# Optimization experiments

Measured on AMD Instinct MI355X. Metric: run time of the kernel, lower is better.

The kernel has to match this reference:

```python
import jax, jax.numpy as jnp
import numpy as np

TOP_K = 2


def setup_inputs() -> dict:
    key = jax.random.key(0)
    k1, k2 = jax.random.split(key)
    hidden_states = jax.random.normal(k1, (4, 8192, 4096), dtype=jnp.float32)
    # xavier_uniform for Linear(4096 -> 64): bound = sqrt(6/(fan_in+fan_out))
    bound = float(np.sqrt(6.0 / (4096 + 64)))
    gate_w = jax.random.uniform(k2, (64, 4096), dtype=jnp.float32, minval=-bound, maxval=bound)
    return {"hidden_states": hidden_states, "gate_w": gate_w}


def reference(hidden_states, gate_w):
    # Flatten [B, S, H] -> [T, H]
    H = hidden_states.shape[-1]
    x = hidden_states.reshape(-1, H)
    # Gate projection: [T, H] @ [H, E] -> [T, E]
    router_logits = jnp.einsum('th,eh->te', x, gate_w)
    # Top-k expert selection (eval mode: no noise)
    top_k_logits, top_k_indices = jax.lax.top_k(router_logits, TOP_K)
    # Normalize selected weights with a softmax over the k logits
    top_k_weights = jax.nn.softmax(top_k_logits, axis=-1)
    return top_k_weights, top_k_indices, router_logits
```

## Files before the change

kernel.cpp:

```cpp
#include <hip/hip_runtime.h>


#define NT    512
#define TT    32768
#define HD    4096
#define NE    64
#define BKT   32
#define NKT   128
#define KCH   2
#define NCH   (NKT / KCH)
#define BROWS 128
#define LDSBUF_U4 1536

typedef __attribute__((ext_vector_type(8))) short bf16x8;
typedef __attribute__((ext_vector_type(4))) float f32x4;

#define MFMA __builtin_amdgcn_mfma_f32_16x16x32_bf16

__device__ __forceinline__ bf16x8 u2b(uint4 u) {
  return __builtin_bit_cast(bf16x8, u);
}

__device__ __forceinline__ void tsplit8(float4 a, float4 b,
                                        uint4& o0, uint4& o1, uint4& o2) {
  float f[8] = {a.x, a.y, a.z, a.w, b.x, b.y, b.z, b.w};
  unsigned p0[4], p1[4], p2[4];
#pragma unroll
  for (int j = 0; j < 4; ++j) {
    float x0 = f[2 * j], x1 = f[2 * j + 1];
    unsigned u0 = __float_as_uint(x0) & 0xffff0000u;
    unsigned u1 = __float_as_uint(x1) & 0xffff0000u;
    float r0 = x0 - __uint_as_float(u0);
    float r1 = x1 - __uint_as_float(u1);
    unsigned v0 = __float_as_uint(r0) & 0xffff0000u;
    unsigned v1 = __float_as_uint(r1) & 0xffff0000u;
    float s0 = r0 - __uint_as_float(v0);
    float s1 = r1 - __uint_as_float(v1);
    p0[j] = (u0 >> 16) | u1;
    p1[j] = (v0 >> 16) | v1;
    p2[j] = (__float_as_uint(s0) >> 16) | (__float_as_uint(s1) & 0xffff0000u);
  }
  o0 = make_uint4(p0[0], p0[1], p0[2], p0[3]);
  o1 = make_uint4(p1[0], p1[1], p1[2], p1[3]);
  o2 = make_uint4(p2[0], p2[1], p2[2], p2[3]);
}

__global__ __launch_bounds__(256)
void prepack_w_kernel(const float* __restrict__ W, uint4* __restrict__ Bp) {
  const int t  = blockIdx.x * 256 + threadIdx.x;
  const int e  = t >> 9;
  const int c8 = t & 511;
  const int k0 = c8 * 8;
  const float4* wp = (const float4*)(W + (size_t)e * HD + k0);
  uint4 o0, o1, o2;
  tsplit8(wp[0], wp[1], o0, o1, o2);
  const int ts = k0 >> 5;
  const int lg = (k0 >> 3) & 3;
  const int f  = e >> 4;
  const int ln = lg * 16 + (e & 15);
  Bp[(((ts * 3 + 0) * 4 + f) << 6) + ln] = o0;
  Bp[(((ts * 3 + 1) * 4 + f) << 6) + ln] = o1;
  Bp[(((ts * 3 + 2) * 4 + f) << 6) + ln] = o2;
}

__global__ __launch_bounds__(NT, 2)
void router_frag_kernel(const float* __restrict__ A, const uint4* __restrict__ Bp,
                        float* __restrict__ outw, float* __restrict__ outi,
                        float* __restrict__ outl) {
  __shared__ __align__(16) uint4 smem[2 * LDSBUF_U4];

  const int tid  = threadIdx.x;
  const int bm   = blockIdx.x;
  const int lane = tid & 63;
  const int w    = tid >> 6;
  const int l15  = lane & 15;
  const int lg   = lane >> 4;

  const int row = bm * BROWS + w * 16 + l15;
  const float* pa = A + (size_t)row * HD + lg * 8;

  const uint4* bsrc = Bp + w * 192 + lane;

  f32x4 acc0 = {0.f,0.f,0.f,0.f}, acc1 = {0.f,0.f,0.f,0.f};
  f32x4 acc2 = {0.f,0.f,0.f,0.f}, acc3 = {0.f,0.f,0.f,0.f};

  uint4 st0, st1, st2;

#define SLOAD(CH) { \
    const uint4* q_ = bsrc + (size_t)(CH) * LDSBUF_U4; \
    st0 = q_[0]; st1 = q_[64]; st2 = q_[128]; }

#define SWRITE(BUFI) { \
    uint4* d_ = smem + (BUFI) * LDSBUF_U4 + w * 192 + lane; \
    d_[0] = st0; d_[64] = st1; d_[128] = st2; }

#define FRAG(T4, F, ACC, A0_, A1_, A2_) { \
    const bf16x8 q0_ = bbx[(((T4) * 3 + 0) * 4 + (F)) * 64 + lane]; \
    const bf16x8 q1_ = bbx[(((T4) * 3 + 1) * 4 + (F)) * 64 + lane]; \
    const bf16x8 q2_ = bbx[(((T4) * 3 + 2) * 4 + (F)) * 64 + lane]; \
    ACC = MFMA(A0_, q2_, ACC, 0, 0, 0); \
    ACC = MFMA(A1_, q1_, ACC, 0, 0, 0); \
    ACC = MFMA(A2_, q0_, ACC, 0, 0, 0); \
    ACC = MFMA(A0_, q1_, ACC, 0, 0, 0); \
    ACC = MFMA(A1_, q0_, ACC, 0, 0, 0); \
    ACC = MFMA(A0_, q0_, ACC, 0, 0, 0); }

#define STEP(T4, AX0, AX1, AY0, AY1) { \
    int tn_ = t0s + (T4) + 1; if (tn_ >= NKT) tn_ = NKT - 1; \
    const float4* ap_ = (const float4*)(pa + (size_t)tn_ * BKT); \
    AY0 = ap_[0]; AY1 = ap_[1]; \
    uint4 x0_, x1_, x2_; \
    tsplit8(AX0, AX1, x0_, x1_, x2_); \
    const bf16x8 a0_ = u2b(x0_), a1_ = u2b(x1_), a2_ = u2b(x2_); \
    FRAG(T4, 0, acc0, a0_, a1_, a2_) \
    FRAG(T4, 1, acc1, a0_, a1_, a2_) \
    FRAG(T4, 2, acc2, a0_, a1_, a2_) \
    FRAG(T4, 3, acc3, a0_, a1_, a2_) }

  SLOAD(0)
  SWRITE(0)
  float4 aX0, aX1, aY0, aY1;
  { const float4* ap = (const float4*)pa; aX0 = ap[0]; aX1 = ap[1]; }
  __syncthreads();

#pragma unroll 1
  for (int c = 0; c < NCH; ++c) {
    const bf16x8* bbx = (const bf16x8*)(smem + (c & 1) * LDSBUF_U4);
    const int t0s = c * KCH;
    const bool more = (c + 1 < NCH);
    if (more) { SLOAD(c + 1) }
    __builtin_amdgcn_sched_barrier(0);
    STEP(0, aX0, aX1, aY0, aY1)
    STEP(1, aY0, aY1, aX0, aX1)
    if (more) { SWRITE((c + 1) & 1) }
    __syncthreads();
  }

  const int tb = bm * BROWS;
  float* lf = (float*)smem;
  const int rbase = w * 16 + lg * 4;

#define EPO(F, ACC) { \
    _Pragma("unroll") \
    for (int r = 0; r < 4; ++r) { \
      int tl = rbase + r; int e = (F) * 16 + l15; float v = ACC[r]; \
      outl[(size_t)(tb + tl) * NE + e] = v; \
      lf[tl * 65 + e] = v; \
    } }
  EPO(0, acc0) EPO(1, acc1) EPO(2, acc2) EPO(3, acc3)
#undef EPO

  __syncthreads();

  if (tid < BROWS) {
    const int t = tid;
    float m1 = -1e30f, m2 = -1e30f;
    int i1 = 0, i2 = 0;
#pragma unroll
    for (int e = 0; e < NE; ++e) {
      float v = lf[t * 65 + e];
      if (v > m1)      { m2 = m1; i2 = i1; m1 = v; i1 = e; }
      else if (v > m2) { m2 = v; i2 = e; }
    }
    float e2  = expf(m2 - m1);
    float inv = 1.0f / (1.0f + e2);
    outw[(size_t)(tb + t) * 2 + 0] = inv;
    outw[(size_t)(tb + t) * 2 + 1] = e2 * inv;
    outi[(size_t)(tb + t) * 2 + 0] = (float)i1;
    outi[(size_t)(tb + t) * 2 + 1] = (float)i2;
  }
}

#define PROD1(AM0, AM1, BS0, BS1) \
    acc00 = MFMA(AM0, BS0, acc00, 0, 0, 0); \
    acc01 = MFMA(AM0, BS1, acc01, 0, 0, 0); \
    acc10 = MFMA(AM1, BS0, acc10, 0, 0, 0); \
    acc11 = MFMA(AM1, BS1, acc11, 0, 0, 0);

__global__ __launch_bounds__(256, 2)
void topk_router_lds(const float* __restrict__ A, const float* __restrict__ W,
                     float* __restrict__ outw, float* __restrict__ outi,
                     float* __restrict__ outl) {
  __shared__ __align__(16) unsigned char smem[49152];
  const int tid  = threadIdx.x;
  const int bm   = blockIdx.x;
  const int lane = tid & 63;
  const int wid  = tid >> 6;
  const int wr   = wid >> 1;
  const int wc   = wid & 1;
  const int l15  = lane & 15;
  const int lg   = lane >> 4;
  const int s_r  = tid >> 2;
  const int s_cb = (tid & 3) << 3;
  const float* aball = A + (size_t)(bm * 64 + s_r) * HD + s_cb;
  const float* bball = W + (size_t)s_r * HD + s_cb;
  const unsigned wswz  = ((unsigned)((s_r >> 1) & 3)) << 4;
  const unsigned wbyte = (unsigned)(s_r * 64) + (((unsigned)(s_cb * 2)) ^ wswz);
  f32x4 acc00 = {0.f,0.f,0.f,0.f}, acc01 = {0.f,0.f,0.f,0.f};
  f32x4 acc10 = {0.f,0.f,0.f,0.f}, acc11 = {0.f,0.f,0.f,0.f};
  float4 aE0, aE1, bE0, bE1, aO0, aO1, bO0, bO1;
#define LOADS(T, A0, A1, B0, B1) { \
    const float4* ap = (const float4*)(aball + (size_t)(T) * BKT); \
    A0 = ap[0]; A1 = ap[1]; \
    const float4* bp = (const float4*)(bball + (size_t)(T) * BKT); \
    B0 = bp[0]; B1 = bp[1]; }
#define CONVW2(BB, A0, A1, B0, B1) { \
    uint4 o0, o1, o2; \
    tsplit8(A0, A1, o0, o1, o2); \
    *(uint4*)(smem + (BB) +     0 + wbyte) = o0; \
    *(uint4*)(smem + (BB) +  4096 + wbyte) = o1; \
    *(uint4*)(smem + (BB) +  8192 + wbyte) = o2; \
    tsplit8(B0, B1, o0, o1, o2); \
    *(uint4*)(smem + (BB) + 12288 + wbyte) = o0; \
    *(uint4*)(smem + (BB) + 16384 + wbyte) = o1; \
    *(uint4*)(smem + (BB) + 20480 + wbyte) = o2; }
  auto compute = [&](int bb) {
    bf16x8 a0m0, a0m1, a1m0, a1m1, a2m0, a2m1;
    bf16x8 b0n0, b0n1, b1n0, b1n1, b2n0, b2n1;
    const unsigned kb = (unsigned)(lg * 16);
#define LDA(SI, MI, DST) { \
    int row = wr * 32 + (MI) * 16 + l15; \
    DST = *(const bf16x8*)(smem + bb + (SI) * 4096 + row * 64 + \
          (kb ^ ((((unsigned)row >> 1) & 3) << 4))); }
#define LDB(SI, NI, DST) { \
    int row = wc * 32 + (NI) * 16 + l15; \
    DST = *(const bf16x8*)(smem + bb + 12288 + (SI) * 4096 + row * 64 + \
          (kb ^ ((((unsigned)row >> 1) & 3) << 4))); }
    LDA(0, 0, a0m0) LDA(0, 1, a0m1)
    LDA(1, 0, a1m0) LDA(1, 1, a1m1)
    LDA(2, 0, a2m0) LDA(2, 1, a2m1)
    LDB(0, 0, b0n0) LDB(0, 1, b0n1)
    LDB(1, 0, b1n0) LDB(1, 1, b1n1)
    LDB(2, 0, b2n0) LDB(2, 1, b2n1)
#undef LDA
#undef LDB
    PROD1(a0m0, a0m1, b2n0, b2n1)
    PROD1(a1m0, a1m1, b1n0, b1n1)
    PROD1(a2m0, a2m1, b0n0, b0n1)
    PROD1(a0m0, a0m1, b1n0, b1n1)
    PROD1(a1m0, a1m1, b0n0, b0n1)
    PROD1(a0m0, a0m1, b0n0, b0n1)
  };
  LOADS(0, aE0, aE1, bE0, bE1)
  LOADS(1, aO0, aO1, bO0, bO1)
  CONVW2(0, aE0, aE1, bE0, bE1)
  __syncthreads();
#pragma unroll 1
  for (int kk = 0; kk < NKT; kk += 2) {
    if (kk + 2 < NKT) { LOADS(kk + 2, aE0, aE1, bE0, bE1) }
    __builtin_amdgcn_sched_barrier(0);
    compute(0);
    CONVW2(24576, aO0, aO1, bO0, bO1)
    __syncthreads();
    if (kk + 3 < NKT) { LOADS(kk + 3, aO0, aO1, bO0, bO1) }
    __builtin_amdgcn_sched_barrier(0);
    compute(24576);
    if (kk + 2 < NKT) { CONVW2(0, aE0, aE1, bE0, bE1) }
    __syncthreads();
  }
  const int t0 = bm * 64;
  float* lf2 = (float*)smem;
#define EPI(MI, NI, ACC) \
  { _Pragma("unroll") \
    for (int r = 0; r < 4; ++r) { \
      int tl = wr * 32 + (MI) * 16 + lg * 4 + r; \
      int e  = wc * 32 + (NI) * 16 + l15; \
      float v = ACC[r]; \
      outl[(size_t)(t0 + tl) * NE + e] = v; \
      lf2[tl * 65 + e] = v; \
    } }
  EPI(0, 0, acc00) EPI(0, 1, acc01) EPI(1, 0, acc10) EPI(1, 1, acc11)
#undef EPI
  __syncthreads();
  if (tid < 64) {
    const int t = tid;
    float m1 = -1e30f, m2 = -1e30f;
    int i1 = 0, i2 = 0;
#pragma unroll
    for (int e = 0; e < NE; ++e) {
      float v = lf2[t * 65 + e];
      if (v > m1)      { m2 = m1; i2 = i1; m1 = v; i1 = e; }
      else if (v > m2) { m2 = v; i2 = e; }
    }
    float e2  = expf(m2 - m1);
    float inv = 1.0f / (1.0f + e2);
    outw[(size_t)(t0 + t) * 2 + 0] = inv;
    outw[(size_t)(t0 + t) * 2 + 1] = e2 * inv;
    outi[(size_t)(t0 + t) * 2 + 0] = (float)i1;
    outi[(size_t)(t0 + t) * 2 + 1] = (float)i2;
  }
}

extern "C" void kernel_launch(void* const* d_in, const int* in_sizes, int n_in,
                              void* d_out, int out_size, void* d_ws, size_t ws_size,
                              hipStream_t stream) {
  (void)in_sizes; (void)n_in; (void)out_size;
  const float* A = (const float*)d_in[0];
  const float* W = (const float*)d_in[1];
  float* outw = (float*)d_out;
  float* outi = (float*)d_out + 2 * TT;
  float* outl = (float*)d_out + 4 * TT;

  const size_t need = (size_t)NKT * 3 * 4 * 1024;
  if (ws_size >= need) {
    hipLaunchKernelGGL(prepack_w_kernel, dim3(128), dim3(256), 0, stream,
                       W, (uint4*)d_ws);
    hipLaunchKernelGGL(router_frag_kernel, dim3(TT / BROWS), dim3(NT), 0, stream,
                       A, (const uint4*)d_ws, outw, outi, outl);
  } else {
    hipLaunchKernelGGL(topk_router_lds, dim3(TT / 64), dim3(256), 0, stream,
                       A, W, outw, outi, outl);
  }
}
```

Baseline: 197.5 us.

## Stream activations into LDS via global_load_lds DMA with 2x2 warp tiling

Replaces the per-wave direct-register activation loads with asynchronous global-to-LDS DMA of 64-row activation tiles, double-buffered in LDS. The weight fragments now come straight from global memory into registers, and each wave computes a 32x32 output tile. The goal is to overlap the HBM streaming of activations with MFMA work and to cut the register-staging overhead. In exchange the block shrinks to 256 threads with 64 rows, padded LDS rows and more complex addressing, and the bf16x3 split moves to data read from LDS.

```diff
diff --git a/kernel.cpp b/kernel.cpp
--- a/kernel.cpp
+++ b/kernel.cpp
@@ -1,24 +1,27 @@
 #include <hip/hip_runtime.h>
 
 
-#define NT    512
+#define NT    256
 #define TT    32768
 #define HD    4096
 #define NE    64
 #define BKT   32
 #define NKT   128
-#define KCH   2
-#define NCH   (NKT / KCH)
-#define BROWS 128
-#define LDSBUF_U4 1536
+#define BUFB  25600
+#define ALIM  ((size_t)TT * HD * 4 - 16)
 
 typedef __attribute__((ext_vector_type(8))) short bf16x8;
 typedef __attribute__((ext_vector_type(4))) float f32x4;
 
 #define MFMA __builtin_amdgcn_mfma_f32_16x16x32_bf16
 
-__device__ __forceinline__ bf16x8 u2b(uint4 u) {
-  return __builtin_bit_cast(bf16x8, u);
+__device__ __forceinline__ bf16x8 u2b(uint4 u) { return __builtin_bit_cast(bf16x8, u); }
+__device__ __forceinline__ float4 b4f(uint4 u) { return __builtin_bit_cast(float4, u); }
+
+__device__ __forceinline__ void gload_lds16(const void* g, void* l) {
+  __builtin_amdgcn_global_load_lds(
+      (const __attribute__((address_space(1))) void*)g,
+      (__attribute__((address_space(3))) void*)l, 16, 0, 0);
 }
 
 __device__ __forceinline__ void tsplit8(float4 a, float4 b,
@@ -49,8 +52,7 @@
 void prepack_w_kernel(const float* __restrict__ W, uint4* __restrict__ Bp) {
   const int t  = blockIdx.x * 256 + threadIdx.x;
   const int e  = t >> 9;
-  const int c8 = t & 511;
-  const int k0 = c8 * 8;
+  const int k0 = (t & 511) * 8;
   const float4* wp = (const float4*)(W + (size_t)e * HD + k0);
   uint4 o0, o1, o2;
   tsplit8(wp[0], wp[1], o0, o1, o2);
@@ -63,96 +65,128 @@
   Bp[(((ts * 3 + 2) * 4 + f) << 6) + ln] = o2;
 }
 
+#define PROD1(AM0, AM1, BN0, BN1) \
+    acc00 = MFMA(AM0, BN0, acc00, 0, 0, 0); \
+    acc01 = MFMA(AM0, BN1, acc01, 0, 0, 0); \
+    acc10 = MFMA(AM1, BN0, acc10, 0, 0, 0); \
+    acc11 = MFMA(AM1, BN1, acc11, 0, 0, 0);
+
 __global__ __launch_bounds__(NT, 2)
-void router_frag_kernel(const float* __restrict__ A, const uint4* __restrict__ Bp,
-                        float* __restrict__ outw, float* __restrict__ outi,
-                        float* __restrict__ outl) {
-  __shared__ __align__(16) uint4 smem[2 * LDSBUF_U4];
+void router_dma_kernel(const float* __restrict__ A, const uint4* __restrict__ Bp,
+                       float* __restrict__ outw, float* __restrict__ outi,
+                       float* __restrict__ outl) {
+  __shared__ __align__(16) unsigned char smem[2 * BUFB];
 
   const int tid  = threadIdx.x;
   const int bm   = blockIdx.x;
   const int lane = tid & 63;
   const int w    = tid >> 6;
+  const int wr   = w >> 1;
+  const int wc   = w & 1;
   const int l15  = lane & 15;
   const int lg   = lane >> 4;
 
-  const int row = bm * BROWS + w * 16 + l15;
-  const float* pa = A + (size_t)row * HD + lg * 8;
-
-  const uint4* bsrc = Bp + w * 192 + lane;
-
-  f32x4 acc0 = {0.f,0.f,0.f,0.f}, acc1 = {0.f,0.f,0.f,0.f};
-  f32x4 acc2 = {0.f,0.f,0.f,0.f}, acc3 = {0.f,0.f,0.f,0.f};
-
-  uint4 st0, st1, st2;
-
-#define SLOAD(CH) { \
-    const uint4* q_ = bsrc + (size_t)(CH) * LDSBUF_U4; \
-    st0 = q_[0]; st1 = q_[64]; st2 = q_[128]; }
-
-#define SWRITE(BUFI) { \
-    uint4* d_ = smem + (BUFI) * LDSBUF_U4 + w * 192 + lane; \
-    d_[0] = st0; d_[64] = st1; d_[128] = st2; }
-
-#define FRAG(T4, F, ACC, A0_, A1_, A2_) { \
-    const bf16x8 q0_ = bbx[(((T4) * 3 + 0) * 4 + (F)) * 64 + lane]; \
-    const bf16x8 q1_ = bbx[(((T4) * 3 + 1) * 4 + (F)) * 64 + lane]; \
-    const bf16x8 q2_ = bbx[(((T4) * 3 + 2) * 4 + (F)) * 64 + lane]; \
-    ACC = MFMA(A0_, q2_, ACC, 0, 0, 0); \
-    ACC = MFMA(A1_, q1_, ACC, 0, 0, 0); \
-    ACC = MFMA(A2_, q0_, ACC, 0, 0, 0); \
-    ACC = MFMA(A0_, q1_, ACC, 0, 0, 0); \
-    ACC = MFMA(A1_, q0_, ACC, 0, 0, 0); \
-    ACC = MFMA(A0_, q0_, ACC, 0, 0, 0); }
-
-#define STEP(T4, AX0, AX1, AY0, AY1) { \
-    int tn_ = t0s + (T4) + 1; if (tn_ >= NKT) tn_ = NKT - 1; \
-    const float4* ap_ = (const float4*)(pa + (size_t)tn_ * BKT); \
-    AY0 = ap_[0]; AY1 = ap_[1]; \
-    uint4 x0_, x1_, x2_; \
-    tsplit8(AX0, AX1, x0_, x1_, x2_); \
-    const bf16x8 a0_ = u2b(x0_), a1_ = u2b(x1_), a2_ = u2b(x2_); \
-    FRAG(T4, 0, acc0, a0_, a1_, a2_) \
-    FRAG(T4, 1, acc1, a0_, a1_, a2_) \
-    FRAG(T4, 2, acc2, a0_, a1_, a2_) \
-    FRAG(T4, 3, acc3, a0_, a1_, a2_) }
-
-  SLOAD(0)
-  SWRITE(0)
-  float4 aX0, aX1, aY0, aY1;
-  { const float4* ap = (const float4*)pa; aX0 = ap[0]; aX1 = ap[1]; }
+  const char* Abytes = (const char*)A;
+
+  size_t srcoff[7];
+#pragma unroll
+  for (int j = 0; j < 7; ++j) {
+    int ii = j * 4 + w;
+    int f  = ii * 1024 + lane * 16;
+    int r  = f / 400, rb = f % 400;
+    srcoff[j] = (size_t)(bm * 64 + r) * (HD * 4) + (size_t)(rb < 384 ? rb : 0);
+  }
+
+#define DMA_ISSUE(CT, BOFF) { \
+    _Pragma("unroll") \
+    for (int j = 0; j < 7; ++j) { \
+      int ii = j * 4 + w; \
+      if (ii < 25) { \
+        size_t off = srcoff[j] + (size_t)(CT) * 384; \
+        if (off > ALIM) off -= (size_t)(HD * 4); \
+        gload_lds16(Abytes + off, smem + (BOFF) + ii * 1024); \
+      } \
+    } \
+    __builtin_amdgcn_sched_barrier(0); }
+
+  const int row0b = (wr * 32 + l15) * 400;
+  const int row1b = row0b + 16 * 400;
+  const int lgb   = lg * 32;
+
+  const uint4* pbB = Bp + wc * 128 + lane;
+
+  f32x4 acc00 = {0.f,0.f,0.f,0.f}, acc01 = {0.f,0.f,0.f,0.f};
+  f32x4 acc10 = {0.f,0.f,0.f,0.f}, acc11 = {0.f,0.f,0.f,0.f};
+
+  uint4 bA0f0, bA0f1, bA1f0, bA1f1, bA2f0, bA2f1;
+  uint4 bB0f0, bB0f1, bB1f0, bB1f1, bB2f0, bB2f1;
+
+#define LOADB(SET, G) { \
+    const uint4* q_ = pbB + (size_t)(G) * 768; \
+    SET##0f0 = q_[0];   SET##0f1 = q_[64]; \
+    SET##1f0 = q_[256]; SET##1f1 = q_[320]; \
+    SET##2f0 = q_[512]; SET##2f1 = q_[576]; }
+
+#define BSTEP(BOFF, S, BU, BL, GN, DOLOAD) { \
+    if (DOLOAD) { LOADB(BL, GN) } \
+    uint4 rA0lo = *(const uint4*)(smem + (BOFF) + row0b + (S) * 128 + lgb); \
+    uint4 rA0hi = *(const uint4*)(smem + (BOFF) + row0b + (S) * 128 + lgb + 16); \
+    uint4 rA1lo = *(const uint4*)(smem + (BOFF) + row1b + (S) * 128 + lgb); \
+    uint4 rA1hi = *(const uint4*)(smem + (BOFF) + row1b + (S) * 128 + lgb + 16); \
+    uint4 x0, x1, x2, y0, y1, y2; \
+    tsplit8(b4f(rA0lo), b4f(rA0hi), x0, x1, x2); \
+    tsplit8(b4f(rA1lo), b4f(rA1hi), y0, y1, y2); \
+    const bf16x8 a0m0 = u2b(x0), a1m0 = u2b(x1), a2m0 = u2b(x2); \
+    const bf16x8 a0m1 = u2b(y0), a1m1 = u2b(y1), a2m1 = u2b(y2); \
+    PROD1(a0m0, a0m1, u2b(BU##2f0), u2b(BU##2f1)) \
+    PROD1(a1m0, a1m1, u2b(BU##1f0), u2b(BU##1f1)) \
+    PROD1(a2m0, a2m1, u2b(BU##0f0), u2b(BU##0f1)) \
+    PROD1(a0m0, a0m1, u2b(BU##1f0), u2b(BU##1f1)) \
+    PROD1(a1m0, a1m1, u2b(BU##0f0), u2b(BU##0f1)) \
+    PROD1(a0m0, a0m1, u2b(BU##0f0), u2b(BU##0f1)) }
+
+  DMA_ISSUE(0, 0)
+  LOADB(bA, 0)
   __syncthreads();
 
 #pragma unroll 1
-  for (int c = 0; c < NCH; ++c) {
-    const bf16x8* bbx = (const bf16x8*)(smem + (c & 1) * LDSBUF_U4);
-    const int t0s = c * KCH;
-    const bool more = (c + 1 < NCH);
-    if (more) { SLOAD(c + 1) }
-    __builtin_amdgcn_sched_barrier(0);
-    STEP(0, aX0, aX1, aY0, aY1)
-    STEP(1, aY0, aY1, aX0, aX1)
-    if (more) { SWRITE((c + 1) & 1) }
+  for (int ot = 0; ot < 21; ++ot) {
+    const int g0 = ot * 6;
+    DMA_ISSUE(2 * ot + 1, BUFB)
+    BSTEP(0, 0, bA, bB, g0 + 1, true)
+    BSTEP(0, 1, bB, bA, g0 + 2, true)
+    BSTEP(0, 2, bA, bB, g0 + 3, true)
     __syncthreads();
-  }
-
-  const int tb = bm * BROWS;
+    DMA_ISSUE(2 * ot + 2, 0)
+    BSTEP(BUFB, 0, bB, bA, g0 + 4, true)
+    BSTEP(BUFB, 1, bA, bB, g0 + 5, true)
+    BSTEP(BUFB, 2, bB, bA, g0 + 6, true)
+    __syncthreads();
+  }
+
+  BSTEP(0, 0, bA, bB, 127, true)
+  BSTEP(0, 1, bB, bA, 0, false)
+
+  const int t0 = bm * 64;
   float* lf = (float*)smem;
-  const int rbase = w * 16 + lg * 4;
-
-#define EPO(F, ACC) { \
-    _Pragma("unroll") \
+
+  __syncthreads();
+
+#define EPO(MI, NI, ACC) \
+  { _Pragma("unroll") \
     for (int r = 0; r < 4; ++r) { \
-      int tl = rbase + r; int e = (F) * 16 + l15; float v = ACC[r]; \
-      outl[(size_t)(tb + tl) * NE + e] = v; \
+      int tl = wr * 32 + (MI) * 16 + lg * 4 + r; \
+      int e  = wc * 32 + (NI) * 16 + l15; \
+      float v = ACC[r]; \
+      outl[(size_t)(t0 + tl) * NE + e] = v; \
       lf[tl * 65 + e] = v; \
     } }
-  EPO(0, acc0) EPO(1, acc1) EPO(2, acc2) EPO(3, acc3)
+  EPO(0, 0, acc00) EPO(0, 1, acc01) EPO(1, 0, acc10) EPO(1, 1, acc11)
 #undef EPO
 
   __syncthreads();
 
-  if (tid < BROWS) {
+  if (tid < 64) {
     const int t = tid;
     float m1 = -1e30f, m2 = -1e30f;
     int i1 = 0, i2 = 0;
@@ -164,18 +198,12 @@
     }
     float e2  = expf(m2 - m1);
     float inv = 1.0f / (1.0f + e2);
-    outw[(size_t)(tb + t) * 2 + 0] = inv;
-    outw[(size_t)(tb + t) * 2 + 1] = e2 * inv;
-    outi[(size_t)(tb + t) * 2 + 0] = (float)i1;
-    outi[(size_t)(tb + t) * 2 + 1] = (float)i2;
-  }
-}
-
-#define PROD1(AM0, AM1, BS0, BS1) \
-    acc00 = MFMA(AM0, BS0, acc00, 0, 0, 0); \
-    acc01 = MFMA(AM0, BS1, acc01, 0, 0, 0); \
-    acc10 = MFMA(AM1, BS0, acc10, 0, 0, 0); \
-    acc11 = MFMA(AM1, BS1, acc11, 0, 0, 0);
+    outw[(size_t)(t0 + t) * 2 + 0] = inv;
+    outw[(size_t)(t0 + t) * 2 + 1] = e2 * inv;
+    outi[(size_t)(t0 + t) * 2 + 0] = (float)i1;
+    outi[(size_t)(t0 + t) * 2 + 1] = (float)i2;
+  }
+}
 
 __global__ __launch_bounds__(256, 2)
 void topk_router_lds(const float* __restrict__ A, const float* __restrict__ W,
@@ -305,7 +333,7 @@
   if (ws_size >= need) {
     hipLaunchKernelGGL(prepack_w_kernel, dim3(128), dim3(256), 0, stream,
                        W, (uint4*)d_ws);
-    hipLaunchKernelGGL(router_frag_kernel, dim3(TT / BROWS), dim3(NT), 0, stream,
+    hipLaunchKernelGGL(router_dma_kernel, dim3(TT / 64), dim3(NT), 0, stream,
                        A, (const uint4*)d_ws, outw, outi, outl);
   } else {
     hipLaunchKernelGGL(topk_router_lds, dim3(TT / 64), dim3(256), 0, stream,
```

After: 172.5 us. -12.7%, faster.
